# Performance work log

Hardware: AMD Instinct MI355X
Metric: run time of the kernel (lower is better)

Reference implementation:

```python
import jax, jax.numpy as jnp
import numpy as np
from jax import lax

K = 3            # oscillators
SUBSTEPS = 4     # fixed RK4 substeps per t_eval interval (replaces adaptive dopri5)
LN_EPS = 1e-5


def setup_inputs() -> dict:
    key = jax.random.key(0)
    ks = jax.random.split(key, 12)
    B, T, H, OH = 32768, 48, 32, 16
    S = 2 * K
    g = lambda k, shp, s: (jax.random.normal(k, shp, dtype=jnp.float32) * s)
    return {
        'expr': jax.random.normal(ks[0], (B, T), dtype=jnp.float32),
        't_eval': jnp.arange(T, dtype=jnp.float32) * 2.0,  # 0..94h, 2h sampling
        'enc_w1': g(ks[1], (T, H), 1.0 / np.sqrt(T)), 'enc_b1': jnp.zeros((H,), jnp.float32),
        'ln_g': jnp.ones((H,), jnp.float32), 'ln_b': jnp.zeros((H,), jnp.float32),
        'enc_w2': g(ks[2], (H, H), 1.0 / np.sqrt(H)), 'enc_b2': jnp.zeros((H,), jnp.float32),
        'enc_w3': g(ks[3], (H, S), 0.1 / np.sqrt(H)), 'enc_b3': jnp.zeros((S,), jnp.float32),
        'periods': jnp.array([24.0, 12.0, 8.0], jnp.float32),
        'gamma': jnp.full((K,), 0.01, jnp.float32),
        'ode_w1': g(ks[4], (S, OH), 0.05), 'ode_b1': jnp.zeros((OH,), jnp.float32),
        'ode_w2': g(ks[5], (OH, S), 0.05), 'ode_b2': jnp.zeros((S,), jnp.float32),
        'dec_w': jnp.ones((K,), jnp.float32) + g(ks[6], (K,), 0.05),
        'dec_b': jnp.float32(0.0),
        'baseline': jnp.float32(0.0),
    }


def _gelu(x):
    return jax.nn.gelu(x, approximate=False)


def _encoder(x, w1, b1, lg, lb, w2, b2, w3, b3):
    h = x @ w1 + b1
    mu = h.mean(-1, keepdims=True)
    var = ((h - mu) ** 2).mean(-1, keepdims=True)
    h = (h - mu) * lax.rsqrt(var + LN_EPS) * lg + lb
    h = _gelu(h)
    h = _gelu(h @ w2 + b2)
    return h @ w3 + b3  # (B, 2K); dropout = identity at eval


def _ode_deriv(z, omega2, gamma, w1, b1, w2, b2):
    # z: (B, 2K) interleaved [x0, v0, x1, v1, ...]
    x = z[..., 0::2]
    v = z[..., 1::2]
    dv = -omega2 * x - 2.0 * gamma * v
    base = jnp.stack([v, dv], axis=-1).reshape(z.shape)
    corr = jnp.tanh(z @ w1 + b1) @ w2 + b2  # tiny residual correction MLP
    return base + corr


def _integrate(z0, t_eval, omega2, gamma, w1, b1, w2, b2):
    f = lambda z: _ode_deriv(z, omega2, gamma, w1, b1, w2, b2)
    dts = jnp.diff(t_eval)

    def interval(z, dt):
        h = dt / SUBSTEPS
        def sub(zc, _):
            k1 = f(zc)
            k2 = f(zc + 0.5 * h * k1)
            k3 = f(zc + 0.5 * h * k2)
            k4 = f(zc + h * k3)
            return zc + (h / 6.0) * (k1 + 2.0 * k2 + 2.0 * k3 + k4), None
        z, _ = lax.scan(sub, z, None, length=SUBSTEPS)
        return z, z

    _, traj_rest = lax.scan(interval, z0, dts)
    return jnp.concatenate([z0[None], traj_rest], axis=0)  # (T, B, 2K)


def reference(expr, t_eval, enc_w1, enc_b1, ln_g, ln_b, enc_w2, enc_b2, enc_w3, enc_b3,
              periods, gamma, ode_w1, ode_b1, ode_w2, ode_b2, dec_w, dec_b, baseline):
    z0 = _encoder(expr, enc_w1, enc_b1, ln_g, ln_b, enc_w2, enc_b2, enc_w3, enc_b3)
    omega = 2.0 * jnp.pi / periods
    traj = _integrate(z0, t_eval, omega ** 2, gamma, ode_w1, ode_b1, ode_w2, ode_b2)
    disp = traj[:, :, 0::2]                       # (T, B, K)
    expr_hat = (disp * dec_w).sum(-1) + dec_b     # linear decoder, (T, B)
    expr_hat = expr_hat.T + baseline              # (B, T)
    amplitudes = jnp.sqrt((disp ** 2).mean(axis=0))  # (B, K)
    return expr_hat, traj, amplitudes
```

## Files before the change

### kernel.cpp

```cpp
#include <hip/hip_runtime.h>
#include <math.h>

#define NB 32768
#define NT 48
#define NH 32
#define NOH 16
#define NK 3
#define NS 6
#define NSUB 4

typedef float f2 __attribute__((ext_vector_type(2)));

#define PIN_V(x) asm volatile("" : "+v"(x))
__device__ __forceinline__ float uni(float x) {
    return __int_as_float(__builtin_amdgcn_readfirstlane(__float_as_int(x)));
}

#define PK_FMA_LO(acc, zp, w) \
    asm("v_pk_fma_f32 %0, %1, %2, %0 op_sel:[0,0,0] op_sel_hi:[0,1,1]" \
        : "+v"(acc) : "v"(zp), "v"(w))
#define PK_FMA_HI(acc, zp, w) \
    asm("v_pk_fma_f32 %0, %1, %2, %0 op_sel:[1,0,0] op_sel_hi:[1,1,1]" \
        : "+v"(acc) : "v"(zp), "v"(w))
#define PK_FMA_LO_I(dst, zp, w, c) \
    asm("v_pk_fma_f32 %0, %1, %2, %3 op_sel:[0,0,0] op_sel_hi:[0,1,1]" \
        : "=v"(dst) : "v"(zp), "v"(w), "v"(c))
#define PK_FMA_SWAP_I(dst, zp, cc, c) \
    asm("v_pk_fma_f32 %0, %1, %2, %3 op_sel:[1,0,0] op_sel_hi:[0,1,1]" \
        : "=v"(dst) : "v"(zp), "v"(cc), "v"(c))

__device__ __forceinline__ f2 fma2(f2 a, f2 b, f2 c) {
    return __builtin_elementwise_fma(a, b, c);
}
__device__ __forceinline__ f2 bc2(float x) { f2 r; r.x = x; r.y = x; return r; }

__device__ __forceinline__ float dpp_xor1(float v) {
    int x = __builtin_amdgcn_update_dpp(0, __float_as_int(v), 0xB1, 0xF, 0xF, false);
    return __int_as_float(x);
}
__device__ __forceinline__ float dpp_xor2(float v) {
    int x = __builtin_amdgcn_update_dpp(0, __float_as_int(v), 0x4E, 0xF, 0xF, false);
    return __int_as_float(x);
}
__device__ __forceinline__ float dpp_xor3(float v) {
    int x = __builtin_amdgcn_update_dpp(0, __float_as_int(v), 0x1B, 0xF, 0xF, false);
    return __int_as_float(x);
}
__device__ __forceinline__ float qsum4(float v) {
    float a = v + dpp_xor1(v);
    return a + dpp_xor2(a);
}

__device__ __forceinline__ float gelu_exact(float x) {
    return 0.5f * x * (1.0f + erff(x * 0.70710678118654752440f));
}

__global__ void __launch_bounds__(256, 2) pinod_kernel(
    const float* __restrict__ expr,
    const float* __restrict__ t_eval,
    const float* __restrict__ enc_w1,
    const float* __restrict__ enc_b1,
    const float* __restrict__ ln_g,
    const float* __restrict__ ln_b,
    const float* __restrict__ enc_w2,
    const float* __restrict__ enc_b2,
    const float* __restrict__ enc_w3,
    const float* __restrict__ enc_b3,
    const float* __restrict__ periods,
    const float* __restrict__ gammav,
    const float* __restrict__ ode_w1,
    const float* __restrict__ ode_b1,
    const float* __restrict__ ode_w2,
    const float* __restrict__ ode_b2,
    const float* __restrict__ dec_w,
    const float* __restrict__ dec_b,
    const float* __restrict__ baseline,
    float* __restrict__ out)
{
    const int tid   = blockIdx.x * 256 + threadIdx.x;
    const int sub   = tid & 3;
    const int b     = tid >> 2;
    const int base8 = sub * 8;
    const int obase = sub * 4;

    float* out_eh  = out;
    float* out_tr  = out + (size_t)NB * NT;
    float* out_amp = out + (size_t)NB * NT + (size_t)NT * NB * NS;

    const float C = 2.88539008177792681472f;

    f2 w1p[NS][2];
    #pragma unroll
    for (int i = 0; i < NS; ++i) {
        float4 wA = *(const float4*)(ode_w1 + i * NOH + obase);
        w1p[i][0].x = C * wA.x; w1p[i][0].y = C * wA.y;
        w1p[i][1].x = C * wA.z; w1p[i][1].y = C * wA.w;
    }
    f2 b1p[2];
    {
        float4 wA = *(const float4*)(ode_b1 + obase);
        b1p[0].x = C * wA.x; b1p[0].y = C * wA.y;
        b1p[1].x = C * wA.z; b1p[1].y = C * wA.w;
    }
    f2 w2p[4][3];
    f2 hb2p[3];
    #pragma unroll
    for (int s = 0; s < 3; ++s) {
        float2 w = *(const float2*)(ode_b2 + 2 * s);
        hb2p[s].x = 0.25f * w.x; hb2p[s].y = 0.25f * w.y;
    }
    #pragma unroll
    for (int j = 0; j < 4; ++j) {
        const float2* wp = (const float2*)(ode_w2 + (obase + j) * NS);
        #pragma unroll
        for (int s = 0; s < 3; ++s) {
            float2 w = wp[s];
            hb2p[s].x += w.x;          hb2p[s].y += w.y;
            w2p[j][s].x = -2.0f * w.x; w2p[j][s].y = -2.0f * w.y;
        }
    }
    f2 c1p[3], c2p[3];
    float dw[NK];
    #pragma unroll
    for (int k = 0; k < NK; ++k) {
        float w = 6.28318530717958647693f / uni(periods[k]);
        c1p[k].x = 1.0f; c1p[k].y = uni(-(w * w));
        c2p[k].x = 0.0f; c2p[k].y = uni(-2.0f * gammav[k]);
        dw[k]    = uni(dec_w[k]);
    }
    const float addc = uni(dec_b[0] + baseline[0]);

    #pragma unroll
    for (int i = 0; i < NS; ++i)
        #pragma unroll
        for (int p = 0; p < 2; ++p) PIN_V(w1p[i][p]);
    #pragma unroll
    for (int p = 0; p < 2; ++p) PIN_V(b1p[p]);
    #pragma unroll
    for (int j = 0; j < 4; ++j)
        #pragma unroll
        for (int s = 0; s < 3; ++s) PIN_V(w2p[j][s]);
    #pragma unroll
    for (int s = 0; s < 3; ++s) { PIN_V(hb2p[s]); PIN_V(c1p[s]); PIN_V(c2p[s]); }

    float h1r[8];
    {
        float4 bv0 = *(const float4*)(enc_b1 + base8);
        float4 bv1 = *(const float4*)(enc_b1 + base8 + 4);
        h1r[0] = bv0.x; h1r[1] = bv0.y; h1r[2] = bv0.z; h1r[3] = bv0.w;
        h1r[4] = bv1.x; h1r[5] = bv1.y; h1r[6] = bv1.z; h1r[7] = bv1.w;
    }
    const float4* xp = (const float4*)(expr + (size_t)b * NT);
    #pragma unroll 1
    for (int t4 = 0; t4 < NT / 4; ++t4) {
        float4 xq = xp[t4];
        float xs[4] = {xq.x, xq.y, xq.z, xq.w};
        #pragma unroll
        for (int u4 = 0; u4 < 4; ++u4) {
            const float* wr = enc_w1 + (t4 * 4 + u4) * NH + base8;
            float x = xs[u4];
            float4 w0 = *(const float4*)(wr);
            float4 w1 = *(const float4*)(wr + 4);
            h1r[0] = fmaf(x, w0.x, h1r[0]); h1r[1] = fmaf(x, w0.y, h1r[1]);
            h1r[2] = fmaf(x, w0.z, h1r[2]); h1r[3] = fmaf(x, w0.w, h1r[3]);
            h1r[4] = fmaf(x, w1.x, h1r[4]); h1r[5] = fmaf(x, w1.y, h1r[5]);
            h1r[6] = fmaf(x, w1.z, h1r[6]); h1r[7] = fmaf(x, w1.w, h1r[7]);
        }
    }
    {
        float s = 0.f;
        #pragma unroll
        for (int u = 0; u < 8; ++u) s += h1r[u];
        float mu = qsum4(s) * (1.0f / NH);
        float v = 0.f;
        #pragma unroll
        for (int u = 0; u < 8; ++u) { float d = h1r[u] - mu; v = fmaf(d, d, v); }
        float var = qsum4(v) * (1.0f / NH);
        float rstd = rsqrtf(var + 1e-5f);
        float4 g0 = *(const float4*)(ln_g + base8);
        float4 g1 = *(const float4*)(ln_g + base8 + 4);
        float4 l0 = *(const float4*)(ln_b + base8);
        float4 l1 = *(const float4*)(ln_b + base8 + 4);
        h1r[0] = gelu_exact((h1r[0] - mu) * rstd * g0.x + l0.x);
        h1r[1] = gelu_exact((h1r[1] - mu) * rstd * g0.y + l0.y);
        h1r[2] = gelu_exact((h1r[2] - mu) * rstd * g0.z + l0.z);
        h1r[3] = gelu_exact((h1r[3] - mu) * rstd * g0.w + l0.w);
        h1r[4] = gelu_exact((h1r[4] - mu) * rstd * g1.x + l1.x);
        h1r[5] = gelu_exact((h1r[5] - mu) * rstd * g1.y + l1.y);
        h1r[6] = gelu_exact((h1r[6] - mu) * rstd * g1.z + l1.z);
        h1r[7] = gelu_exact((h1r[7] - mu) * rstd * g1.w + l1.w);
    }
    float acc[8];
    {
        float4 bv0 = *(const float4*)(enc_b2 + base8);
        float4 bv1 = *(const float4*)(enc_b2 + base8 + 4);
        acc[0] = bv0.x; acc[1] = bv0.y; acc[2] = bv0.z; acc[3] = bv0.w;
        acc[4] = bv1.x; acc[5] = bv1.y; acc[6] = bv1.z; acc[7] = bv1.w;
    }
    #pragma unroll 1
    for (int u = 0; u < 8; ++u) {
        float mine = h1r[u];
        float o1   = dpp_xor1(mine);
        float o2   = dpp_xor2(mine);
        float o3   = dpp_xor3(mine);
        const float* wr0 = enc_w2 + (base8 + u) * NH + base8;
        const float* wr1 = enc_w2 + ((base8 ^ 8) + u) * NH + base8;
        const float* wr2 = enc_w2 + ((base8 ^ 16) + u) * NH + base8;
        const float* wr3 = enc_w2 + ((base8 ^ 24) + u) * NH + base8;
        float4 a0 = *(const float4*)(wr0), a1 = *(const float4*)(wr0 + 4);
        float4 b0 = *(const float4*)(wr1), b1 = *(const float4*)(wr1 + 4);
        float4 c0 = *(const float4*)(wr2), c1 = *(const float4*)(wr2 + 4);
        float4 d0 = *(const float4*)(wr3), d1 = *(const float4*)(wr3 + 4);
        acc[0] = fmaf(mine, a0.x, fmaf(o1, b0.x, fmaf(o2, c0.x, fmaf(o3, d0.x, acc[0]))));
        acc[1] = fmaf(mine, a0.y, fmaf(o1, b0.y, fmaf(o2, c0.y, fmaf(o3, d0.y, acc[1]))));
        acc[2] = fmaf(mine, a0.z, fmaf(o1, b0.z, fmaf(o2, c0.z, fmaf(o3, d0.z, acc[2]))));
        acc[3] = fmaf(mine, a0.w, fmaf(o1, b0.w, fmaf(o2, c0.w, fmaf(o3, d0.w, acc[3]))));
        acc[4] = fmaf(mine, a1.x, fmaf(o1, b1.x, fmaf(o2, c1.x, fmaf(o3, d1.x, acc[4]))));
        acc[5] = fmaf(mine, a1.y, fmaf(o1, b1.y, fmaf(o2, c1.y, fmaf(o3, d1.y, acc[5]))));
        acc[6] = fmaf(mine, a1.z, fmaf(o1, b1.z, fmaf(o2, c1.z, fmaf(o3, d1.z, acc[6]))));
        acc[7] = fmaf(mine, a1.w, fmaf(o1, b1.w, fmaf(o2, c1.w, fmaf(o3, d1.w, acc[7]))));
    }
    f2 z[3];
    {
        float zp[NS] = {0.f, 0.f, 0.f, 0.f, 0.f, 0.f};
        #pragma unroll 1
        for (int u = 0; u < 8; ++u) {
            float gm = gelu_exact(acc[u]);
            const float2* wp = (const float2*)(enc_w3 + (base8 + u) * NS);
            float2 w0 = wp[0], w1 = wp[1], w2 = wp[2];
            zp[0] = fmaf(gm, w0.x, zp[0]); zp[1] = fmaf(gm, w0.y, zp[1]);
            zp[2] = fmaf(gm, w1.x, zp[2]); zp[3] = fmaf(gm, w1.y, zp[3]);
            zp[4] = fmaf(gm, w2.x, zp[4]); zp[5] = fmaf(gm, w2.y, zp[5]);
        }
        #pragma unroll
        for (int s = 0; s < 3; ++s) {
            z[s].x = qsum4(zp[2 * s])     + enc_b3[2 * s];
            z[s].y = qsum4(zp[2 * s + 1]) + enc_b3[2 * s + 1];
        }
    }

    auto deriv = [&](const f2 (&zz)[3], f2 (&d)[3]) {
        f2 a[2];
        #pragma unroll
        for (int p = 0; p < 2; ++p) {
            PK_FMA_LO_I(a[p], zz[0], w1p[0][p], b1p[p]);
            PK_FMA_HI (a[p], zz[0], w1p[1][p]);
        }
        #pragma unroll
        for (int s = 1; s < 3; ++s) {
            #pragma unroll
            for (int p = 0; p < 2; ++p) {
                PK_FMA_LO(a[p], zz[s], w1p[2 * s][p]);
                PK_FMA_HI(a[p], zz[s], w1p[2 * s + 1][p]);
            }
        }
        f2 rc[2];
        #pragma unroll
        for (int p = 0; p < 2; ++p) {
            f2 e; e.x = __builtin_amdgcn_exp2f(a[p].x); e.y = __builtin_amdgcn_exp2f(a[p].y);
            f2 r = e + bc2(1.0f);
            rc[p].x = __builtin_amdgcn_rcpf(r.x); rc[p].y = __builtin_amdgcn_rcpf(r.y);
        }
        f2 pd[3];
        #pragma unroll
        for (int s = 0; s < 3; ++s) {
            PK_FMA_LO_I(pd[s], rc[0], w2p[0][s], hb2p[s]);
            PK_FMA_HI (pd[s], rc[0], w2p[1][s]);
            PK_FMA_LO (pd[s], rc[1], w2p[2][s]);
            PK_FMA_HI (pd[s], rc[1], w2p[3][s]);
        }
        #pragma unroll
        for (int s = 0; s < 3; ++s) {
            f2 o;
            o.x = dpp_xor1(pd[s].x); o.y = dpp_xor1(pd[s].y);
            pd[s] += o;
            o.x = dpp_xor2(pd[s].x); o.y = dpp_xor2(pd[s].y);
            pd[s] += o;
            f2 t;
            PK_FMA_SWAP_I(t, zz[s], c1p[s], pd[s]);
            d[s] = fma2(zz[s], c2p[s], t);
        }
    };

    float amp[NK];
    {
        float eh = addc;
        #pragma unroll
        for (int k = 0; k < NK; ++k) {
            float xx = z[k].x;
            amp[k] = xx * xx;
            eh = fmaf(xx, dw[k], eh);
        }
        float* tp = out_tr + (size_t)b * NS;
        if (sub == 3) {
            out_eh[(size_t)b * NT] = eh;
        } else {
            f2 zsel = (sub == 0) ? z[0] : ((sub == 1) ? z[1] : z[2]);
            float2 sv = {zsel.x, zsel.y};
            *(float2*)(tp + 2 * sub) = sv;
        }
    }

    float te_prev = t_eval[0];
    #pragma unroll 1
    for (int t = 1; t < NT; ++t) {
        const float te  = t_eval[t];
        const float dt  = te - te_prev;
        te_prev = te;
        const float hh  = dt * (1.0f / NSUB);
        const float hh2 = 0.5f * hh;
        const float hh6 = hh * (1.0f / 6.0f);
        f2 hh2p = bc2(hh2), hhp = bc2(hh), hh6p = bc2(hh6);
        #pragma unroll 1
        for (int ss = 0; ss < NSUB; ++ss) {
            f2 d[3], zt[3], zs[3];
            deriv(z, d);
            #pragma unroll
            for (int s = 0; s < 3; ++s) { zs[s] = d[s]; zt[s] = fma2(hh2p, d[s], z[s]); }
            deriv(zt, d);
            #pragma unroll
            for (int s = 0; s < 3; ++s) { zs[s] = fma2(bc2(2.f), d[s], zs[s]); zt[s] = fma2(hh2p, d[s], z[s]); }
            deriv(zt, d);
            #pragma unroll
            for (int s = 0; s < 3; ++s) { zs[s] = fma2(bc2(2.f), d[s], zs[s]); zt[s] = fma2(hhp, d[s], z[s]); }
            deriv(zt, d);
            #pragma unroll
            for (int s = 0; s < 3; ++s) z[s] = fma2(hh6p, zs[s] + d[s], z[s]);
        }
        float eh = addc;
        #pragma unroll
        for (int k = 0; k < NK; ++k) {
            float xx = z[k].x;
            amp[k] = fmaf(xx, xx, amp[k]);
            eh = fmaf(xx, dw[k], eh);
        }
        float* tp = out_tr + ((size_t)t * NB + b) * NS;
        if (sub == 3) {
            out_eh[(size_t)b * NT + t] = eh;
        } else {
            f2 zsel = (sub == 0) ? z[0] : ((sub == 1) ? z[1] : z[2]);
            float2 sv = {zsel.x, zsel.y};
            *(float2*)(tp + 2 * sub) = sv;
        }
    }

    if (sub < 3) {
        float av = (sub == 0) ? amp[0] : ((sub == 1) ? amp[1] : amp[2]);
        out_amp[(size_t)b * NK + sub] = sqrtf(av * (1.0f / NT));
    }
}

extern "C" void kernel_launch(void* const* d_in, const int* in_sizes, int n_in,
                              void* d_out, int out_size, void* d_ws, size_t ws_size,
                              hipStream_t stream) {
    pinod_kernel<<<(NB * 4) / 256, 256, 0, stream>>>(
        (const float*)d_in[0],  (const float*)d_in[1],  (const float*)d_in[2],
        (const float*)d_in[3],  (const float*)d_in[4],  (const float*)d_in[5],
        (const float*)d_in[6],  (const float*)d_in[7],  (const float*)d_in[8],
        (const float*)d_in[9],  (const float*)d_in[10], (const float*)d_in[11],
        (const float*)d_in[12], (const float*)d_in[13], (const float*)d_in[14],
        (const float*)d_in[15], (const float*)d_in[16], (const float*)d_in[17],
        (const float*)d_in[18], (float*)d_out);
}
```

Baseline: 347.4 us.

## Process two batch elements per thread group to interleave independent RK4 chains

Each 4-lane group now encodes and integrates two batch rows, interleaving their derivative evaluations so two independent dependency chains can overlap within a wave. The grid is halved and launch bounds are relaxed to one block per SIMD pair, allowing more registers per thread. The goal is to hide ALU and DPP latency with instruction-level parallelism instead of more waves. In exchange, each SIMD holds far fewer waves, and register pressure roughly doubles for the state.

```diff
diff --git a/kernel.cpp b/kernel.cpp
--- a/kernel.cpp
+++ b/kernel.cpp
@@ -55,7 +55,7 @@
     return 0.5f * x * (1.0f + erff(x * 0.70710678118654752440f));
 }
 
-__global__ void __launch_bounds__(256, 2) pinod_kernel(
+__global__ void __launch_bounds__(256, 1) pinod_kernel(
     const float* __restrict__ expr,
     const float* __restrict__ t_eval,
     const float* __restrict__ enc_w1,
@@ -79,7 +79,9 @@
 {
     const int tid   = blockIdx.x * 256 + threadIdx.x;
     const int sub   = tid & 3;
-    const int b     = tid >> 2;
+    const int pair  = tid >> 2;
+    const int bA    = pair * 2;
+    const int bB    = bA + 1;
     const int base8 = sub * 8;
     const int obase = sub * 4;
 
@@ -143,101 +145,106 @@
     #pragma unroll
     for (int s = 0; s < 3; ++s) { PIN_V(hb2p[s]); PIN_V(c1p[s]); PIN_V(c2p[s]); }
 
-    float h1r[8];
-    {
-        float4 bv0 = *(const float4*)(enc_b1 + base8);
-        float4 bv1 = *(const float4*)(enc_b1 + base8 + 4);
-        h1r[0] = bv0.x; h1r[1] = bv0.y; h1r[2] = bv0.z; h1r[3] = bv0.w;
-        h1r[4] = bv1.x; h1r[5] = bv1.y; h1r[6] = bv1.z; h1r[7] = bv1.w;
-    }
-    const float4* xp = (const float4*)(expr + (size_t)b * NT);
-    #pragma unroll 1
-    for (int t4 = 0; t4 < NT / 4; ++t4) {
-        float4 xq = xp[t4];
-        float xs[4] = {xq.x, xq.y, xq.z, xq.w};
-        #pragma unroll
-        for (int u4 = 0; u4 < 4; ++u4) {
-            const float* wr = enc_w1 + (t4 * 4 + u4) * NH + base8;
-            float x = xs[u4];
-            float4 w0 = *(const float4*)(wr);
-            float4 w1 = *(const float4*)(wr + 4);
-            h1r[0] = fmaf(x, w0.x, h1r[0]); h1r[1] = fmaf(x, w0.y, h1r[1]);
-            h1r[2] = fmaf(x, w0.z, h1r[2]); h1r[3] = fmaf(x, w0.w, h1r[3]);
-            h1r[4] = fmaf(x, w1.x, h1r[4]); h1r[5] = fmaf(x, w1.y, h1r[5]);
-            h1r[6] = fmaf(x, w1.z, h1r[6]); h1r[7] = fmaf(x, w1.w, h1r[7]);
-        }
-    }
-    {
-        float s = 0.f;
-        #pragma unroll
-        for (int u = 0; u < 8; ++u) s += h1r[u];
-        float mu = qsum4(s) * (1.0f / NH);
-        float v = 0.f;
-        #pragma unroll
-        for (int u = 0; u < 8; ++u) { float d = h1r[u] - mu; v = fmaf(d, d, v); }
-        float var = qsum4(v) * (1.0f / NH);
-        float rstd = rsqrtf(var + 1e-5f);
-        float4 g0 = *(const float4*)(ln_g + base8);
-        float4 g1 = *(const float4*)(ln_g + base8 + 4);
-        float4 l0 = *(const float4*)(ln_b + base8);
-        float4 l1 = *(const float4*)(ln_b + base8 + 4);
-        h1r[0] = gelu_exact((h1r[0] - mu) * rstd * g0.x + l0.x);
-        h1r[1] = gelu_exact((h1r[1] - mu) * rstd * g0.y + l0.y);
-        h1r[2] = gelu_exact((h1r[2] - mu) * rstd * g0.z + l0.z);
-        h1r[3] = gelu_exact((h1r[3] - mu) * rstd * g0.w + l0.w);
-        h1r[4] = gelu_exact((h1r[4] - mu) * rstd * g1.x + l1.x);
-        h1r[5] = gelu_exact((h1r[5] - mu) * rstd * g1.y + l1.y);
-        h1r[6] = gelu_exact((h1r[6] - mu) * rstd * g1.z + l1.z);
-        h1r[7] = gelu_exact((h1r[7] - mu) * rstd * g1.w + l1.w);
-    }
-    float acc[8];
-    {
-        float4 bv0 = *(const float4*)(enc_b2 + base8);
-        float4 bv1 = *(const float4*)(enc_b2 + base8 + 4);
-        acc[0] = bv0.x; acc[1] = bv0.y; acc[2] = bv0.z; acc[3] = bv0.w;
-        acc[4] = bv1.x; acc[5] = bv1.y; acc[6] = bv1.z; acc[7] = bv1.w;
-    }
-    #pragma unroll 1
-    for (int u = 0; u < 8; ++u) {
-        float mine = h1r[u];
-        float o1   = dpp_xor1(mine);
-        float o2   = dpp_xor2(mine);
-        float o3   = dpp_xor3(mine);
-        const float* wr0 = enc_w2 + (base8 + u) * NH + base8;
-        const float* wr1 = enc_w2 + ((base8 ^ 8) + u) * NH + base8;
-        const float* wr2 = enc_w2 + ((base8 ^ 16) + u) * NH + base8;
-        const float* wr3 = enc_w2 + ((base8 ^ 24) + u) * NH + base8;
-        float4 a0 = *(const float4*)(wr0), a1 = *(const float4*)(wr0 + 4);
-        float4 b0 = *(const float4*)(wr1), b1 = *(const float4*)(wr1 + 4);
-        float4 c0 = *(const float4*)(wr2), c1 = *(const float4*)(wr2 + 4);
-        float4 d0 = *(const float4*)(wr3), d1 = *(const float4*)(wr3 + 4);
-        acc[0] = fmaf(mine, a0.x, fmaf(o1, b0.x, fmaf(o2, c0.x, fmaf(o3, d0.x, acc[0]))));
-        acc[1] = fmaf(mine, a0.y, fmaf(o1, b0.y, fmaf(o2, c0.y, fmaf(o3, d0.y, acc[1]))));
-        acc[2] = fmaf(mine, a0.z, fmaf(o1, b0.z, fmaf(o2, c0.z, fmaf(o3, d0.z, acc[2]))));
-        acc[3] = fmaf(mine, a0.w, fmaf(o1, b0.w, fmaf(o2, c0.w, fmaf(o3, d0.w, acc[3]))));
-        acc[4] = fmaf(mine, a1.x, fmaf(o1, b1.x, fmaf(o2, c1.x, fmaf(o3, d1.x, acc[4]))));
-        acc[5] = fmaf(mine, a1.y, fmaf(o1, b1.y, fmaf(o2, c1.y, fmaf(o3, d1.y, acc[5]))));
-        acc[6] = fmaf(mine, a1.z, fmaf(o1, b1.z, fmaf(o2, c1.z, fmaf(o3, d1.z, acc[6]))));
-        acc[7] = fmaf(mine, a1.w, fmaf(o1, b1.w, fmaf(o2, c1.w, fmaf(o3, d1.w, acc[7]))));
-    }
-    f2 z[3];
-    {
-        float zp[NS] = {0.f, 0.f, 0.f, 0.f, 0.f, 0.f};
+    auto encode = [&](int b, f2 (&z)[3]) {
+        float h1r[8];
+        {
+            float4 bv0 = *(const float4*)(enc_b1 + base8);
+            float4 bv1 = *(const float4*)(enc_b1 + base8 + 4);
+            h1r[0] = bv0.x; h1r[1] = bv0.y; h1r[2] = bv0.z; h1r[3] = bv0.w;
+            h1r[4] = bv1.x; h1r[5] = bv1.y; h1r[6] = bv1.z; h1r[7] = bv1.w;
+        }
+        const float4* xp = (const float4*)(expr + (size_t)b * NT);
+        #pragma unroll 1
+        for (int t4 = 0; t4 < NT / 4; ++t4) {
+            float4 xq = xp[t4];
+            float xs[4] = {xq.x, xq.y, xq.z, xq.w};
+            #pragma unroll
+            for (int u4 = 0; u4 < 4; ++u4) {
+                const float* wr = enc_w1 + (t4 * 4 + u4) * NH + base8;
+                float x = xs[u4];
+                float4 w0 = *(const float4*)(wr);
+                float4 w1 = *(const float4*)(wr + 4);
+                h1r[0] = fmaf(x, w0.x, h1r[0]); h1r[1] = fmaf(x, w0.y, h1r[1]);
+                h1r[2] = fmaf(x, w0.z, h1r[2]); h1r[3] = fmaf(x, w0.w, h1r[3]);
+                h1r[4] = fmaf(x, w1.x, h1r[4]); h1r[5] = fmaf(x, w1.y, h1r[5]);
+                h1r[6] = fmaf(x, w1.z, h1r[6]); h1r[7] = fmaf(x, w1.w, h1r[7]);
+            }
+        }
+        {
+            float s = 0.f;
+            #pragma unroll
+            for (int u = 0; u < 8; ++u) s += h1r[u];
+            float mu = qsum4(s) * (1.0f / NH);
+            float v = 0.f;
+            #pragma unroll
+            for (int u = 0; u < 8; ++u) { float d = h1r[u] - mu; v = fmaf(d, d, v); }
+            float var = qsum4(v) * (1.0f / NH);
+            float rstd = rsqrtf(var + 1e-5f);
+            float4 g0 = *(const float4*)(ln_g + base8);
+            float4 g1 = *(const float4*)(ln_g + base8 + 4);
+            float4 l0 = *(const float4*)(ln_b + base8);
+            float4 l1 = *(const float4*)(ln_b + base8 + 4);
+            h1r[0] = gelu_exact((h1r[0] - mu) * rstd * g0.x + l0.x);
+            h1r[1] = gelu_exact((h1r[1] - mu) * rstd * g0.y + l0.y);
+            h1r[2] = gelu_exact((h1r[2] - mu) * rstd * g0.z + l0.z);
+            h1r[3] = gelu_exact((h1r[3] - mu) * rstd * g0.w + l0.w);
+            h1r[4] = gelu_exact((h1r[4] - mu) * rstd * g1.x + l1.x);
+            h1r[5] = gelu_exact((h1r[5] - mu) * rstd * g1.y + l1.y);
+            h1r[6] = gelu_exact((h1r[6] - mu) * rstd * g1.z + l1.z);
+            h1r[7] = gelu_exact((h1r[7] - mu) * rstd * g1.w + l1.w);
+        }
+        float acc[8];
+        {
+            float4 bv0 = *(const float4*)(enc_b2 + base8);
+            float4 bv1 = *(const float4*)(enc_b2 + base8 + 4);
+            acc[0] = bv0.x; acc[1] = bv0.y; acc[2] = bv0.z; acc[3] = bv0.w;
+            acc[4] = bv1.x; acc[5] = bv1.y; acc[6] = bv1.z; acc[7] = bv1.w;
+        }
         #pragma unroll 1
         for (int u = 0; u < 8; ++u) {
-            float gm = gelu_exact(acc[u]);
-            const float2* wp = (const float2*)(enc_w3 + (base8 + u) * NS);
-            float2 w0 = wp[0], w1 = wp[1], w2 = wp[2];
-            zp[0] = fmaf(gm, w0.x, zp[0]); zp[1] = fmaf(gm, w0.y, zp[1]);
-            zp[2] = fmaf(gm, w1.x, zp[2]); zp[3] = fmaf(gm, w1.y, zp[3]);
-            zp[4] = fmaf(gm, w2.x, zp[4]); zp[5] = fmaf(gm, w2.y, zp[5]);
-        }
-        #pragma unroll
-        for (int s = 0; s < 3; ++s) {
-            z[s].x = qsum4(zp[2 * s])     + enc_b3[2 * s];
-            z[s].y = qsum4(zp[2 * s + 1]) + enc_b3[2 * s + 1];
-        }
-    }
+            float mine = h1r[u];
+            float o1   = dpp_xor1(mine);
+            float o2   = dpp_xor2(mine);
+            float o3   = dpp_xor3(mine);
+            const float* wr0 = enc_w2 + (base8 + u) * NH + base8;
+            const float* wr1 = enc_w2 + ((base8 ^ 8) + u) * NH + base8;
+            const float* wr2 = enc_w2 + ((base8 ^ 16) + u) * NH + base8;
+            const float* wr3 = enc_w2 + ((base8 ^ 24) + u) * NH + base8;
+            float4 a0 = *(const float4*)(wr0), a1 = *(const float4*)(wr0 + 4);
+            float4 b0 = *(const float4*)(wr1), b1 = *(const float4*)(wr1 + 4);
+            float4 c0 = *(const float4*)(wr2), c1 = *(const float4*)(wr2 + 4);
+            float4 d0 = *(const float4*)(wr3), d1 = *(const float4*)(wr3 + 4);
+            acc[0] = fmaf(mine, a0.x, fmaf(o1, b0.x, fmaf(o2, c0.x, fmaf(o3, d0.x, acc[0]))));
+            acc[1] = fmaf(mine, a0.y, fmaf(o1, b0.y, fmaf(o2, c0.y, fmaf(o3, d0.y, acc[1]))));
+            acc[2] = fmaf(mine, a0.z, fmaf(o1, b0.z, fmaf(o2, c0.z, fmaf(o3, d0.z, acc[2]))));
+            acc[3] = fmaf(mine, a0.w, fmaf(o1, b0.w, fmaf(o2, c0.w, fmaf(o3, d0.w, acc[3]))));
+            acc[4] = fmaf(mine, a1.x, fmaf(o1, b1.x, fmaf(o2, c1.x, fmaf(o3, d1.x, acc[4]))));
+            acc[5] = fmaf(mine, a1.y, fmaf(o1, b1.y, fmaf(o2, c1.y, fmaf(o3, d1.y, acc[5]))));
+            acc[6] = fmaf(mine, a1.z, fmaf(o1, b1.z, fmaf(o2, c1.z, fmaf(o3, d1.z, acc[6]))));
+            acc[7] = fmaf(mine, a1.w, fmaf(o1, b1.w, fmaf(o2, c1.w, fmaf(o3, d1.w, acc[7]))));
+        }
+        {
+            float zp[NS] = {0.f, 0.f, 0.f, 0.f, 0.f, 0.f};
+            #pragma unroll 1
+            for (int u = 0; u < 8; ++u) {
+                float gm = gelu_exact(acc[u]);
+                const float2* wp = (const float2*)(enc_w3 + (base8 + u) * NS);
+                float2 w0 = wp[0], w1 = wp[1], w2 = wp[2];
+                zp[0] = fmaf(gm, w0.x, zp[0]); zp[1] = fmaf(gm, w0.y, zp[1]);
+                zp[2] = fmaf(gm, w1.x, zp[2]); zp[3] = fmaf(gm, w1.y, zp[3]);
+                zp[4] = fmaf(gm, w2.x, zp[4]); zp[5] = fmaf(gm, w2.y, zp[5]);
+            }
+            #pragma unroll
+            for (int s = 0; s < 3; ++s) {
+                z[s].x = qsum4(zp[2 * s])     + enc_b3[2 * s];
+                z[s].y = qsum4(zp[2 * s + 1]) + enc_b3[2 * s + 1];
+            }
+        }
+    };
+
+    f2 zA[3], zB[3];
+    encode(bA, zA);
+    encode(bB, zB);
 
     auto deriv = [&](const f2 (&zz)[3], f2 (&d)[3]) {
         f2 a[2];
@@ -282,24 +289,27 @@
         }
     };
 
-    float amp[NK];
-    {
+    float ampA[NK], ampB[NK];
+    auto emit = [&](int b, const f2 (&z)[3], float (&amp)[NK], int t, bool init) {
         float eh = addc;
         #pragma unroll
         for (int k = 0; k < NK; ++k) {
             float xx = z[k].x;
-            amp[k] = xx * xx;
+            amp[k] = init ? (xx * xx) : fmaf(xx, xx, amp[k]);
             eh = fmaf(xx, dw[k], eh);
         }
-        float* tp = out_tr + (size_t)b * NS;
+        float* tp = out_tr + ((size_t)t * NB + b) * NS;
         if (sub == 3) {
-            out_eh[(size_t)b * NT] = eh;
+            out_eh[(size_t)b * NT + t] = eh;
         } else {
             f2 zsel = (sub == 0) ? z[0] : ((sub == 1) ? z[1] : z[2]);
             float2 sv = {zsel.x, zsel.y};
             *(float2*)(tp + 2 * sub) = sv;
         }
-    }
+    };
+
+    emit(bA, zA, ampA, 0, true);
+    emit(bB, zB, ampB, 0, true);
 
     float te_prev = t_eval[0];
     #pragma unroll 1
@@ -313,47 +323,52 @@
         f2 hh2p = bc2(hh2), hhp = bc2(hh), hh6p = bc2(hh6);
         #pragma unroll 1
         for (int ss = 0; ss < NSUB; ++ss) {
-            f2 d[3], zt[3], zs[3];
-            deriv(z, d);
-            #pragma unroll
-            for (int s = 0; s < 3; ++s) { zs[s] = d[s]; zt[s] = fma2(hh2p, d[s], z[s]); }
-            deriv(zt, d);
-            #pragma unroll
-            for (int s = 0; s < 3; ++s) { zs[s] = fma2(bc2(2.f), d[s], zs[s]); zt[s] = fma2(hh2p, d[s], z[s]); }
-            deriv(zt, d);
-            #pragma unroll
-            for (int s = 0; s < 3; ++s) { zs[s] = fma2(bc2(2.f), d[s], zs[s]); zt[s] = fma2(hhp, d[s], z[s]); }
-            deriv(zt, d);
-            #pragma unroll
-            for (int s = 0; s < 3; ++s) z[s] = fma2(hh6p, zs[s] + d[s], z[s]);
-        }
-        float eh = addc;
-        #pragma unroll
-        for (int k = 0; k < NK; ++k) {
-            float xx = z[k].x;
-            amp[k] = fmaf(xx, xx, amp[k]);
-            eh = fmaf(xx, dw[k], eh);
-        }
-        float* tp = out_tr + ((size_t)t * NB + b) * NS;
-        if (sub == 3) {
-            out_eh[(size_t)b * NT + t] = eh;
-        } else {
-            f2 zsel = (sub == 0) ? z[0] : ((sub == 1) ? z[1] : z[2]);
-            float2 sv = {zsel.x, zsel.y};
-            *(float2*)(tp + 2 * sub) = sv;
-        }
+            f2 dA[3], dB[3], ztA[3], ztB[3], zsA[3], zsB[3];
+            deriv(zA, dA);
+            deriv(zB, dB);
+            #pragma unroll
+            for (int s = 0; s < 3; ++s) {
+                zsA[s] = dA[s]; ztA[s] = fma2(hh2p, dA[s], zA[s]);
+                zsB[s] = dB[s]; ztB[s] = fma2(hh2p, dB[s], zB[s]);
+            }
+            deriv(ztA, dA);
+            deriv(ztB, dB);
+            #pragma unroll
+            for (int s = 0; s < 3; ++s) {
+                zsA[s] = fma2(bc2(2.f), dA[s], zsA[s]); ztA[s] = fma2(hh2p, dA[s], zA[s]);
+                zsB[s] = fma2(bc2(2.f), dB[s], zsB[s]); ztB[s] = fma2(hh2p, dB[s], zB[s]);
+            }
+            deriv(ztA, dA);
+            deriv(ztB, dB);
+            #pragma unroll
+            for (int s = 0; s < 3; ++s) {
+                zsA[s] = fma2(bc2(2.f), dA[s], zsA[s]); ztA[s] = fma2(hhp, dA[s], zA[s]);
+                zsB[s] = fma2(bc2(2.f), dB[s], zsB[s]); ztB[s] = fma2(hhp, dB[s], zB[s]);
+            }
+            deriv(ztA, dA);
+            deriv(ztB, dB);
+            #pragma unroll
+            for (int s = 0; s < 3; ++s) {
+                zA[s] = fma2(hh6p, zsA[s] + dA[s], zA[s]);
+                zB[s] = fma2(hh6p, zsB[s] + dB[s], zB[s]);
+            }
+        }
+        emit(bA, zA, ampA, t, false);
+        emit(bB, zB, ampB, t, false);
     }
 
     if (sub < 3) {
-        float av = (sub == 0) ? amp[0] : ((sub == 1) ? amp[1] : amp[2]);
-        out_amp[(size_t)b * NK + sub] = sqrtf(av * (1.0f / NT));
+        float avA = (sub == 0) ? ampA[0] : ((sub == 1) ? ampA[1] : ampA[2]);
+        float avB = (sub == 0) ? ampB[0] : ((sub == 1) ? ampB[1] : ampB[2]);
+        out_amp[(size_t)bA * NK + sub] = sqrtf(avA * (1.0f / NT));
+        out_amp[(size_t)bB * NK + sub] = sqrtf(avB * (1.0f / NT));
     }
 }
 
 extern "C" void kernel_launch(void* const* d_in, const int* in_sizes, int n_in,
                               void* d_out, int out_size, void* d_ws, size_t ws_size,
                               hipStream_t stream) {
-    pinod_kernel<<<(NB * 4) / 256, 256, 0, stream>>>(
+    pinod_kernel<<<(NB * 2) / 256, 256, 0, stream>>>(
         (const float*)d_in[0],  (const float*)d_in[1],  (const float*)d_in[2],
         (const float*)d_in[3],  (const float*)d_in[4],  (const float*)d_in[5],
         (const float*)d_in[6],  (const float*)d_in[7],  (const float*)d_in[8],
```

Result: slower. 373.3 us (+7.4%).

## Split each sample across two lanes instead of four to halve cross-lane reductions

Applied to the files above, without the earlier changes.

Each batch sample is now handled by 2 threads instead of 4, so every thread owns 8 of the 16 ODE hidden units and 16 of the 32 encoder hidden units. This removes one DPP shuffle-add stage from every derivative evaluation and from the encoder reductions, and reduces the redundant per-lane work on the 6-element state. Accumulators are split into two independent chains to expose ILP. In exchange each thread holds twice the weights and launches half as many threads, which raises register pressure, and the launch bound is relaxed to allow it.

```diff
diff --git a/kernel.cpp b/kernel.cpp
--- a/kernel.cpp
+++ b/kernel.cpp
@@ -25,6 +25,9 @@
 #define PK_FMA_LO_I(dst, zp, w, c) \
     asm("v_pk_fma_f32 %0, %1, %2, %3 op_sel:[0,0,0] op_sel_hi:[0,1,1]" \
         : "=v"(dst) : "v"(zp), "v"(w), "v"(c))
+#define PK_MUL_HI_I(dst, zp, w) \
+    asm("v_pk_mul_f32 %0, %1, %2 op_sel:[1,0] op_sel_hi:[1,1]" \
+        : "=v"(dst) : "v"(zp), "v"(w))
 #define PK_FMA_SWAP_I(dst, zp, cc, c) \
     asm("v_pk_fma_f32 %0, %1, %2, %3 op_sel:[1,0,0] op_sel_hi:[0,1,1]" \
         : "=v"(dst) : "v"(zp), "v"(cc), "v"(c))
@@ -38,24 +41,13 @@
     int x = __builtin_amdgcn_update_dpp(0, __float_as_int(v), 0xB1, 0xF, 0xF, false);
     return __int_as_float(x);
 }
-__device__ __forceinline__ float dpp_xor2(float v) {
-    int x = __builtin_amdgcn_update_dpp(0, __float_as_int(v), 0x4E, 0xF, 0xF, false);
-    return __int_as_float(x);
-}
-__device__ __forceinline__ float dpp_xor3(float v) {
-    int x = __builtin_amdgcn_update_dpp(0, __float_as_int(v), 0x1B, 0xF, 0xF, false);
-    return __int_as_float(x);
-}
-__device__ __forceinline__ float qsum4(float v) {
-    float a = v + dpp_xor1(v);
-    return a + dpp_xor2(a);
-}
+__device__ __forceinline__ float qsum2(float v) { return v + dpp_xor1(v); }
 
 __device__ __forceinline__ float gelu_exact(float x) {
     return 0.5f * x * (1.0f + erff(x * 0.70710678118654752440f));
 }
 
-__global__ void __launch_bounds__(256, 2) pinod_kernel(
+__global__ void __launch_bounds__(256, 1) pinod_kernel(
     const float* __restrict__ expr,
     const float* __restrict__ t_eval,
     const float* __restrict__ enc_w1,
@@ -77,11 +69,11 @@
     const float* __restrict__ baseline,
     float* __restrict__ out)
 {
-    const int tid   = blockIdx.x * 256 + threadIdx.x;
-    const int sub   = tid & 3;
-    const int b     = tid >> 2;
-    const int base8 = sub * 8;
-    const int obase = sub * 4;
+    const int tid    = blockIdx.x * 256 + threadIdx.x;
+    const int sub    = tid & 1;
+    const int b      = tid >> 1;
+    const int base16 = sub * 16;
+    const int obase  = sub * 8;
 
     float* out_eh  = out;
     float* out_tr  = out + (size_t)NB * NT;
@@ -89,28 +81,32 @@
 
     const float C = 2.88539008177792681472f;
 
-    f2 w1p[NS][2];
+    f2 w1p[NS][4];
     #pragma unroll
     for (int i = 0; i < NS; ++i) {
         float4 wA = *(const float4*)(ode_w1 + i * NOH + obase);
+        float4 wB = *(const float4*)(ode_w1 + i * NOH + obase + 4);
         w1p[i][0].x = C * wA.x; w1p[i][0].y = C * wA.y;
         w1p[i][1].x = C * wA.z; w1p[i][1].y = C * wA.w;
-    }
-    f2 b1p[2];
+        w1p[i][2].x = C * wB.x; w1p[i][2].y = C * wB.y;
+        w1p[i][3].x = C * wB.z; w1p[i][3].y = C * wB.w;
+    }
+    f2 b1p[4];
     {
         float4 wA = *(const float4*)(ode_b1 + obase);
-        b1p[0].x = C * wA.x; b1p[0].y = C * wA.y;
-        b1p[1].x = C * wA.z; b1p[1].y = C * wA.w;
-    }
-    f2 w2p[4][3];
+        float4 wB = *(const float4*)(ode_b1 + obase + 4);
+        b1p[0].x = C * wA.x; b1p[0].y = C * wA.y; b1p[1].x = C * wA.z; b1p[1].y = C * wA.w;
+        b1p[2].x = C * wB.x; b1p[2].y = C * wB.y; b1p[3].x = C * wB.z; b1p[3].y = C * wB.w;
+    }
+    f2 w2p[8][3];
     f2 hb2p[3];
     #pragma unroll
     for (int s = 0; s < 3; ++s) {
         float2 w = *(const float2*)(ode_b2 + 2 * s);
-        hb2p[s].x = 0.25f * w.x; hb2p[s].y = 0.25f * w.y;
-    }
-    #pragma unroll
-    for (int j = 0; j < 4; ++j) {
+        hb2p[s].x = 0.5f * w.x; hb2p[s].y = 0.5f * w.y;
+    }
+    #pragma unroll
+    for (int j = 0; j < 8; ++j) {
         const float2* wp = (const float2*)(ode_w2 + (obase + j) * NS);
         #pragma unroll
         for (int s = 0; s < 3; ++s) {
@@ -133,22 +129,21 @@
     #pragma unroll
     for (int i = 0; i < NS; ++i)
         #pragma unroll
-        for (int p = 0; p < 2; ++p) PIN_V(w1p[i][p]);
-    #pragma unroll
-    for (int p = 0; p < 2; ++p) PIN_V(b1p[p]);
-    #pragma unroll
-    for (int j = 0; j < 4; ++j)
+        for (int p = 0; p < 4; ++p) PIN_V(w1p[i][p]);
+    #pragma unroll
+    for (int p = 0; p < 4; ++p) PIN_V(b1p[p]);
+    #pragma unroll
+    for (int j = 0; j < 8; ++j)
         #pragma unroll
         for (int s = 0; s < 3; ++s) PIN_V(w2p[j][s]);
     #pragma unroll
     for (int s = 0; s < 3; ++s) { PIN_V(hb2p[s]); PIN_V(c1p[s]); PIN_V(c2p[s]); }
 
-    float h1r[8];
-    {
-        float4 bv0 = *(const float4*)(enc_b1 + base8);
-        float4 bv1 = *(const float4*)(enc_b1 + base8 + 4);
-        h1r[0] = bv0.x; h1r[1] = bv0.y; h1r[2] = bv0.z; h1r[3] = bv0.w;
-        h1r[4] = bv1.x; h1r[5] = bv1.y; h1r[6] = bv1.z; h1r[7] = bv1.w;
+    float h1r[16];
+    #pragma unroll
+    for (int q = 0; q < 4; ++q) {
+        float4 bv = *(const float4*)(enc_b1 + base16 + 4 * q);
+        h1r[4 * q] = bv.x; h1r[4 * q + 1] = bv.y; h1r[4 * q + 2] = bv.z; h1r[4 * q + 3] = bv.w;
     }
     const float4* xp = (const float4*)(expr + (size_t)b * NT);
     #pragma unroll 1
@@ -157,76 +152,67 @@
         float xs[4] = {xq.x, xq.y, xq.z, xq.w};
         #pragma unroll
         for (int u4 = 0; u4 < 4; ++u4) {
-            const float* wr = enc_w1 + (t4 * 4 + u4) * NH + base8;
+            const float* wr = enc_w1 + (t4 * 4 + u4) * NH + base16;
             float x = xs[u4];
-            float4 w0 = *(const float4*)(wr);
-            float4 w1 = *(const float4*)(wr + 4);
-            h1r[0] = fmaf(x, w0.x, h1r[0]); h1r[1] = fmaf(x, w0.y, h1r[1]);
-            h1r[2] = fmaf(x, w0.z, h1r[2]); h1r[3] = fmaf(x, w0.w, h1r[3]);
-            h1r[4] = fmaf(x, w1.x, h1r[4]); h1r[5] = fmaf(x, w1.y, h1r[5]);
-            h1r[6] = fmaf(x, w1.z, h1r[6]); h1r[7] = fmaf(x, w1.w, h1r[7]);
+            #pragma unroll
+            for (int q = 0; q < 4; ++q) {
+                float4 w = *(const float4*)(wr + 4 * q);
+                h1r[4 * q]     = fmaf(x, w.x, h1r[4 * q]);
+                h1r[4 * q + 1] = fmaf(x, w.y, h1r[4 * q + 1]);
+                h1r[4 * q + 2] = fmaf(x, w.z, h1r[4 * q + 2]);
+                h1r[4 * q + 3] = fmaf(x, w.w, h1r[4 * q + 3]);
+            }
         }
     }
     {
         float s = 0.f;
         #pragma unroll
-        for (int u = 0; u < 8; ++u) s += h1r[u];
-        float mu = qsum4(s) * (1.0f / NH);
+        for (int u = 0; u < 16; ++u) s += h1r[u];
+        float mu = qsum2(s) * (1.0f / NH);
         float v = 0.f;
         #pragma unroll
-        for (int u = 0; u < 8; ++u) { float d = h1r[u] - mu; v = fmaf(d, d, v); }
-        float var = qsum4(v) * (1.0f / NH);
+        for (int u = 0; u < 16; ++u) { float d = h1r[u] - mu; v = fmaf(d, d, v); }
+        float var = qsum2(v) * (1.0f / NH);
         float rstd = rsqrtf(var + 1e-5f);
-        float4 g0 = *(const float4*)(ln_g + base8);
-        float4 g1 = *(const float4*)(ln_g + base8 + 4);
-        float4 l0 = *(const float4*)(ln_b + base8);
-        float4 l1 = *(const float4*)(ln_b + base8 + 4);
-        h1r[0] = gelu_exact((h1r[0] - mu) * rstd * g0.x + l0.x);
-        h1r[1] = gelu_exact((h1r[1] - mu) * rstd * g0.y + l0.y);
-        h1r[2] = gelu_exact((h1r[2] - mu) * rstd * g0.z + l0.z);
-        h1r[3] = gelu_exact((h1r[3] - mu) * rstd * g0.w + l0.w);
-        h1r[4] = gelu_exact((h1r[4] - mu) * rstd * g1.x + l1.x);
-        h1r[5] = gelu_exact((h1r[5] - mu) * rstd * g1.y + l1.y);
-        h1r[6] = gelu_exact((h1r[6] - mu) * rstd * g1.z + l1.z);
-        h1r[7] = gelu_exact((h1r[7] - mu) * rstd * g1.w + l1.w);
-    }
-    float acc[8];
-    {
-        float4 bv0 = *(const float4*)(enc_b2 + base8);
-        float4 bv1 = *(const float4*)(enc_b2 + base8 + 4);
-        acc[0] = bv0.x; acc[1] = bv0.y; acc[2] = bv0.z; acc[3] = bv0.w;
-        acc[4] = bv1.x; acc[5] = bv1.y; acc[6] = bv1.z; acc[7] = bv1.w;
+        #pragma unroll
+        for (int q = 0; q < 4; ++q) {
+            float4 g = *(const float4*)(ln_g + base16 + 4 * q);
+            float4 l = *(const float4*)(ln_b + base16 + 4 * q);
+            h1r[4 * q]     = gelu_exact((h1r[4 * q]     - mu) * rstd * g.x + l.x);
+            h1r[4 * q + 1] = gelu_exact((h1r[4 * q + 1] - mu) * rstd * g.y + l.y);
+            h1r[4 * q + 2] = gelu_exact((h1r[4 * q + 2] - mu) * rstd * g.z + l.z);
+            h1r[4 * q + 3] = gelu_exact((h1r[4 * q + 3] - mu) * rstd * g.w + l.w);
+        }
+    }
+    float acc[16];
+    #pragma unroll
+    for (int q = 0; q < 4; ++q) {
+        float4 bv = *(const float4*)(enc_b2 + base16 + 4 * q);
+        acc[4 * q] = bv.x; acc[4 * q + 1] = bv.y; acc[4 * q + 2] = bv.z; acc[4 * q + 3] = bv.w;
     }
     #pragma unroll 1
-    for (int u = 0; u < 8; ++u) {
-        float mine = h1r[u];
-        float o1   = dpp_xor1(mine);
-        float o2   = dpp_xor2(mine);
-        float o3   = dpp_xor3(mine);
-        const float* wr0 = enc_w2 + (base8 + u) * NH + base8;
-        const float* wr1 = enc_w2 + ((base8 ^ 8) + u) * NH + base8;
-        const float* wr2 = enc_w2 + ((base8 ^ 16) + u) * NH + base8;
-        const float* wr3 = enc_w2 + ((base8 ^ 24) + u) * NH + base8;
-        float4 a0 = *(const float4*)(wr0), a1 = *(const float4*)(wr0 + 4);
-        float4 b0 = *(const float4*)(wr1), b1 = *(const float4*)(wr1 + 4);
-        float4 c0 = *(const float4*)(wr2), c1 = *(const float4*)(wr2 + 4);
-        float4 d0 = *(const float4*)(wr3), d1 = *(const float4*)(wr3 + 4);
-        acc[0] = fmaf(mine, a0.x, fmaf(o1, b0.x, fmaf(o2, c0.x, fmaf(o3, d0.x, acc[0]))));
-        acc[1] = fmaf(mine, a0.y, fmaf(o1, b0.y, fmaf(o2, c0.y, fmaf(o3, d0.y, acc[1]))));
-        acc[2] = fmaf(mine, a0.z, fmaf(o1, b0.z, fmaf(o2, c0.z, fmaf(o3, d0.z, acc[2]))));
-        acc[3] = fmaf(mine, a0.w, fmaf(o1, b0.w, fmaf(o2, c0.w, fmaf(o3, d0.w, acc[3]))));
-        acc[4] = fmaf(mine, a1.x, fmaf(o1, b1.x, fmaf(o2, c1.x, fmaf(o3, d1.x, acc[4]))));
-        acc[5] = fmaf(mine, a1.y, fmaf(o1, b1.y, fmaf(o2, c1.y, fmaf(o3, d1.y, acc[5]))));
-        acc[6] = fmaf(mine, a1.z, fmaf(o1, b1.z, fmaf(o2, c1.z, fmaf(o3, d1.z, acc[6]))));
-        acc[7] = fmaf(mine, a1.w, fmaf(o1, b1.w, fmaf(o2, c1.w, fmaf(o3, d1.w, acc[7]))));
+    for (int u = 0; u < 16; ++u) {
+        float mine  = h1r[u];
+        float other = dpp_xor1(mine);
+        const float* wa = enc_w2 + (base16 + u) * NH + base16;
+        const float* wb = enc_w2 + ((16 - base16) + u) * NH + base16;
+        #pragma unroll
+        for (int q = 0; q < 4; ++q) {
+            float4 w1v = *(const float4*)(wa + 4 * q);
+            float4 w2v = *(const float4*)(wb + 4 * q);
+            acc[4 * q]     = fmaf(mine, w1v.x, fmaf(other, w2v.x, acc[4 * q]));
+            acc[4 * q + 1] = fmaf(mine, w1v.y, fmaf(other, w2v.y, acc[4 * q + 1]));
+            acc[4 * q + 2] = fmaf(mine, w1v.z, fmaf(other, w2v.z, acc[4 * q + 2]));
+            acc[4 * q + 3] = fmaf(mine, w1v.w, fmaf(other, w2v.w, acc[4 * q + 3]));
+        }
     }
     f2 z[3];
     {
         float zp[NS] = {0.f, 0.f, 0.f, 0.f, 0.f, 0.f};
         #pragma unroll 1
-        for (int u = 0; u < 8; ++u) {
+        for (int u = 0; u < 16; ++u) {
             float gm = gelu_exact(acc[u]);
-            const float2* wp = (const float2*)(enc_w3 + (base8 + u) * NS);
+            const float2* wp = (const float2*)(enc_w3 + (base16 + u) * NS);
             float2 w0 = wp[0], w1 = wp[1], w2 = wp[2];
             zp[0] = fmaf(gm, w0.x, zp[0]); zp[1] = fmaf(gm, w0.y, zp[1]);
             zp[2] = fmaf(gm, w1.x, zp[2]); zp[3] = fmaf(gm, w1.y, zp[3]);
@@ -234,50 +220,55 @@
         }
         #pragma unroll
         for (int s = 0; s < 3; ++s) {
-            z[s].x = qsum4(zp[2 * s])     + enc_b3[2 * s];
-            z[s].y = qsum4(zp[2 * s + 1]) + enc_b3[2 * s + 1];
+            z[s].x = qsum2(zp[2 * s])     + enc_b3[2 * s];
+            z[s].y = qsum2(zp[2 * s + 1]) + enc_b3[2 * s + 1];
         }
     }
 
     auto deriv = [&](const f2 (&zz)[3], f2 (&d)[3]) {
-        f2 a[2];
-        #pragma unroll
-        for (int p = 0; p < 2; ++p) {
-            PK_FMA_LO_I(a[p], zz[0], w1p[0][p], b1p[p]);
-            PK_FMA_HI (a[p], zz[0], w1p[1][p]);
+        f2 aA[4], aB[4];
+        #pragma unroll
+        for (int p = 0; p < 4; ++p) {
+            PK_FMA_LO_I(aA[p], zz[0], w1p[0][p], b1p[p]);
+            PK_MUL_HI_I(aB[p], zz[0], w1p[1][p]);
         }
         #pragma unroll
         for (int s = 1; s < 3; ++s) {
             #pragma unroll
-            for (int p = 0; p < 2; ++p) {
-                PK_FMA_LO(a[p], zz[s], w1p[2 * s][p]);
-                PK_FMA_HI(a[p], zz[s], w1p[2 * s + 1][p]);
+            for (int p = 0; p < 4; ++p) {
+                PK_FMA_LO(aA[p], zz[s], w1p[2 * s][p]);
+                PK_FMA_HI(aB[p], zz[s], w1p[2 * s + 1][p]);
             }
         }
-        f2 rc[2];
-        #pragma unroll
-        for (int p = 0; p < 2; ++p) {
-            f2 e; e.x = __builtin_amdgcn_exp2f(a[p].x); e.y = __builtin_amdgcn_exp2f(a[p].y);
+        f2 rc[4];
+        #pragma unroll
+        for (int p = 0; p < 4; ++p) {
+            f2 a = aA[p] + aB[p];
+            f2 e; e.x = __builtin_amdgcn_exp2f(a.x); e.y = __builtin_amdgcn_exp2f(a.y);
             f2 r = e + bc2(1.0f);
             rc[p].x = __builtin_amdgcn_rcpf(r.x); rc[p].y = __builtin_amdgcn_rcpf(r.y);
         }
-        f2 pd[3];
+        f2 pdA[3], pdB[3];
         #pragma unroll
         for (int s = 0; s < 3; ++s) {
-            PK_FMA_LO_I(pd[s], rc[0], w2p[0][s], hb2p[s]);
-            PK_FMA_HI (pd[s], rc[0], w2p[1][s]);
-            PK_FMA_LO (pd[s], rc[1], w2p[2][s]);
-            PK_FMA_HI (pd[s], rc[1], w2p[3][s]);
+            PK_FMA_LO_I(pdA[s], rc[0], w2p[0][s], hb2p[s]);
+            PK_MUL_HI_I(pdB[s], rc[0], w2p[1][s]);
+        }
+        #pragma unroll
+        for (int p = 1; p < 4; ++p) {
+            #pragma unroll
+            for (int s = 0; s < 3; ++s) {
+                PK_FMA_LO(pdA[s], rc[p], w2p[2 * p][s]);
+                PK_FMA_HI(pdB[s], rc[p], w2p[2 * p + 1][s]);
+            }
         }
         #pragma unroll
         for (int s = 0; s < 3; ++s) {
-            f2 o;
-            o.x = dpp_xor1(pd[s].x); o.y = dpp_xor1(pd[s].y);
-            pd[s] += o;
-            o.x = dpp_xor2(pd[s].x); o.y = dpp_xor2(pd[s].y);
-            pd[s] += o;
+            f2 pd = pdA[s] + pdB[s];
+            f2 o; o.x = dpp_xor1(pd.x); o.y = dpp_xor1(pd.y);
+            pd += o;
             f2 t;
-            PK_FMA_SWAP_I(t, zz[s], c1p[s], pd[s]);
+            PK_FMA_SWAP_I(t, zz[s], c1p[s], pd);
             d[s] = fma2(zz[s], c2p[s], t);
         }
     };
@@ -292,12 +283,13 @@
             eh = fmaf(xx, dw[k], eh);
         }
         float* tp = out_tr + (size_t)b * NS;
-        if (sub == 3) {
+        if (sub == 0) {
             out_eh[(size_t)b * NT] = eh;
+            float2 s0 = {z[0].x, z[0].y}, s1 = {z[1].x, z[1].y};
+            *(float2*)tp = s0; *(float2*)(tp + 2) = s1;
         } else {
-            f2 zsel = (sub == 0) ? z[0] : ((sub == 1) ? z[1] : z[2]);
-            float2 sv = {zsel.x, zsel.y};
-            *(float2*)(tp + 2 * sub) = sv;
+            float2 s2 = {z[2].x, z[2].y};
+            *(float2*)(tp + 4) = s2;
         }
     }
 
@@ -335,25 +327,28 @@
             eh = fmaf(xx, dw[k], eh);
         }
         float* tp = out_tr + ((size_t)t * NB + b) * NS;
-        if (sub == 3) {
+        if (sub == 0) {
             out_eh[(size_t)b * NT + t] = eh;
+            float2 s0 = {z[0].x, z[0].y}, s1 = {z[1].x, z[1].y};
+            *(float2*)tp = s0; *(float2*)(tp + 2) = s1;
         } else {
-            f2 zsel = (sub == 0) ? z[0] : ((sub == 1) ? z[1] : z[2]);
-            float2 sv = {zsel.x, zsel.y};
-            *(float2*)(tp + 2 * sub) = sv;
-        }
-    }
-
-    if (sub < 3) {
-        float av = (sub == 0) ? amp[0] : ((sub == 1) ? amp[1] : amp[2]);
-        out_amp[(size_t)b * NK + sub] = sqrtf(av * (1.0f / NT));
+            float2 s2 = {z[2].x, z[2].y};
+            *(float2*)(tp + 4) = s2;
+        }
+    }
+
+    if (sub == 0) {
+        out_amp[(size_t)b * NK]     = sqrtf(amp[0] * (1.0f / NT));
+        out_amp[(size_t)b * NK + 1] = sqrtf(amp[1] * (1.0f / NT));
+    } else {
+        out_amp[(size_t)b * NK + 2] = sqrtf(amp[2] * (1.0f / NT));
     }
 }
 
 extern "C" void kernel_launch(void* const* d_in, const int* in_sizes, int n_in,
                               void* d_out, int out_size, void* d_ws, size_t ws_size,
                               hipStream_t stream) {
-    pinod_kernel<<<(NB * 4) / 256, 256, 0, stream>>>(
+    pinod_kernel<<<(NB * 2) / 256, 256, 0, stream>>>(
         (const float*)d_in[0],  (const float*)d_in[1],  (const float*)d_in[2],
         (const float*)d_in[3],  (const float*)d_in[4],  (const float*)d_in[5],
         (const float*)d_in[6],  (const float*)d_in[7],  (const float*)d_in[8],
```

Result: faster. 291.9 us (-16.0%).
